# Kernel optimization log

Measured on AMD Instinct MI355X. Metric: run time of the kernel, lower is better.

Reference implementation:

```python
import jax, jax.numpy as jnp
import numpy as np

B, C, H, W = 8, 64, 128, 128
E, HEADS, HID = 3, 16, 16  # num experts, attention heads, routing hidden dim


def setup_inputs() -> dict:
    key = jax.random.key(0)
    ks = jax.random.split(key, 8)
    s = 0.05
    return {
        "x": jax.random.normal(ks[0], (B, C, H, W), jnp.float32),
        "hidden": jax.random.normal(ks[1], (B, HID, 1, 1), jnp.float32),
        # per-expert params, stacked along leading expert dim
        "qkv_w": jax.random.normal(ks[2], (E, 3 * C, C), jnp.float32) * s,   # 1x1 conv, no bias
        "dw_w": jax.random.normal(ks[3], (E, C, 1, 3, 3), jnp.float32) * s,  # depthwise 3x3
        "proj_w": jax.random.normal(ks[4], (E, C, C), jnp.float32) * s,      # 1x1 conv, no bias
        "temp": jnp.ones((E, HEADS, 1, 1), jnp.float32),                     # temperature
        # routing module params
        "r1_w": jax.random.normal(ks[5], (HID, C + HID), jnp.float32) * s,
        "r1_b": jnp.zeros((HID,), jnp.float32),
        "r3_w": jax.random.normal(ks[6], (E, HID), jnp.float32) * s,
        "r3_b": jnp.zeros((E,), jnp.float32),
    }


def _l2norm(t):
    # torch F.normalize: x / max(||x||, eps)
    n = jnp.sqrt(jnp.sum(t * t, axis=-1, keepdims=True))
    return t / jnp.maximum(n, 1e-12)


def _expert(x, qkv_w, dw_w, proj_w, temp):
    b, c, h, w = x.shape
    d = c // HEADS
    qkv = jnp.einsum('bchw,oc->bohw', x, qkv_w)  # [b,3c,h,w]
    q, k, v = jnp.split(qkv, 3, axis=1)
    rs = lambda t: t.reshape(b, HEADS, d, h * w)  # b head c (hw)
    q, k, v = _l2norm(rs(q)), _l2norm(rs(k)), rs(v)
    attn = jnp.einsum('bhcn,bhdn->bhcd', q, k) * temp  # tiny [b,head,d,d]
    attn = jax.nn.softmax(attn, axis=-1)
    out = jnp.einsum('bhcd,bhdn->bhcn', attn, v).reshape(b, c, h, w)
    out = jax.lax.conv_general_dilated(
        out, dw_w, window_strides=(1, 1), padding='SAME',
        feature_group_count=c, dimension_numbers=('NCHW', 'OIHW', 'NCHW'))
    return jnp.einsum('bchw,oc->bohw', out, proj_w)


def reference(x, hidden, qkv_w, dw_w, proj_w, temp, r1_w, r1_b, r3_w, r3_b):
    # routing
    x_global = jnp.mean(x, axis=(2, 3), keepdims=True)          # [b,c,1,1]
    cat = jnp.concatenate([x_global, hidden], axis=1)            # [b,c+16,1,1]
    h1 = jnp.einsum('bchw,oc->bohw', cat, r1_w) + r1_b[None, :, None, None]
    hidden_new = jax.nn.gelu(h1, approximate=False)              # [b,16,1,1]
    logit = jax.nn.relu(jnp.einsum('bchw,oc->bohw', hidden_new, r3_w)
                        + r3_b[None, :, None, None])             # [b,E,1,1]
    # dense expert evaluation
    outs = jnp.stack([_expert(x, qkv_w[i], dw_w[i], proj_w[i], temp[i])
                      for i in range(E)], axis=1)                # [b,E,c,h,w]
    logit5 = logit[..., None]                                    # [b,E,1,1,1]
    out = jnp.sum(outs * logit5, axis=1)                         # [b,c,h,w]
    return out, hidden_new, logit5
```

## Files before the change

kernel.cpp:

```cpp
#include <hip/hip_runtime.h>
#include <math.h>


#define OFF_XG    0
#define OFF_COV   512
#define OFF_LOGIT 33280
#define OFF_MV    33312
#define OFF_H_BYTES  526464
#define OFF_XT_BYTES 1116288

#define OUT_HID   8388608
#define OUT_LOGIT 8388736

#define XP 4224
#define HP 584

typedef __attribute__((ext_vector_type(8))) short bf16x8;
typedef __attribute__((ext_vector_type(4))) float f32x4;

__device__ inline unsigned short f2bf(float f) {
    union { float f; unsigned int u; } v; v.f = f;
    return (unsigned short)((v.u + 0x7FFFu + ((v.u >> 16) & 1u)) >> 16);
}
__device__ inline float bf2f(unsigned short h) {
    union { unsigned int u; float f; } v; v.u = ((unsigned int)h) << 16;
    return v.f;
}

__global__ __launch_bounds__(256) void cov_kernel(const float* __restrict__ x,
                                                  float* __restrict__ ws) {
    __shared__ unsigned short xl[64 * 520];
    const int t = threadIdx.x;
    const int w = t >> 6, l = t & 63;
    const int b = blockIdx.x >> 5;
    const int chunk = blockIdx.x & 31;
    const float* xb = x + ((size_t)b << 20) + (chunk << 9);

    for (int i = 0; i < 32; ++i) {
        const int idx = i * 256 + t;
        const int c = idx >> 7, u = idx & 127;
        const float4 v = *(const float4*)(xb + ((size_t)c << 14) + (u << 2));
        unsigned long long pk = (unsigned long long)f2bf(v.x)
                              | ((unsigned long long)f2bf(v.y) << 16)
                              | ((unsigned long long)f2bf(v.z) << 32)
                              | ((unsigned long long)f2bf(v.w) << 48);
        *(unsigned long long*)&xl[c * 520 + (u << 2)] = pk;
    }
    __syncthreads();

    {
        const int c = t & 63, q = t >> 6;
        float s = 0.f;
        for (int u = 0; u < 16; ++u) {
            const unsigned short* p = &xl[c * 520 + q * 128 + u * 8];
            #pragma unroll
            for (int j = 0; j < 8; ++j) s += bf2f(p[j]);
        }
        atomicAdd(ws + OFF_XG + b * 64 + c, s);
    }

    f32x4 acc[10];
    const f32x4 fz = {0.f, 0.f, 0.f, 0.f};
    #pragma unroll
    for (int q = 0; q < 10; ++q) acc[q] = fz;

    const int lane_a = (l & 15) * 520 + (l >> 4) * 8;
    #pragma unroll
    for (int ks = 0; ks < 4; ++ks) {
        const int p0 = w * 128 + ks * 32;
        bf16x8 fr[4];
        #pragma unroll
        for (int mi = 0; mi < 4; ++mi)
            fr[mi] = *(const bf16x8*)&xl[mi * 16 * 520 + p0 + lane_a];
        int q = 0;
        #pragma unroll
        for (int mi = 0; mi < 4; ++mi)
            #pragma unroll
            for (int ni = mi; ni < 4; ++ni) {
                acc[q] = __builtin_amdgcn_mfma_f32_16x16x32_bf16(fr[mi], fr[ni], acc[q], 0, 0, 0);
                ++q;
            }
    }

    {
        unsigned short* xtw = (unsigned short*)((char*)ws + OFF_XT_BYTES)
                            + ((size_t)b << 20) + ((size_t)(chunk << 9) << 6);
        for (int p = t; p < 512; p += 256) {
            #pragma unroll
            for (int i = 0; i < 8; ++i) {
                bf16x8 v;
                #pragma unroll
                for (int k = 0; k < 8; ++k) v[k] = (short)xl[(i * 8 + k) * 520 + p];
                *(bf16x8*)&xtw[((size_t)p << 6) + (i << 3)] = v;
            }
        }
    }
    __syncthreads();

    float* red = (float*)xl;
    #pragma unroll
    for (int q = 0; q < 10; ++q)
        #pragma unroll
        for (int j = 0; j < 4; ++j)
            red[w * 2560 + q * 256 + ((l >> 4) * 4 + j) * 16 + (l & 15)] = acc[q][j];
    __syncthreads();

    const int MI[10] = {0,0,0,0,1,1,1,2,2,3};
    const int NI[10] = {0,1,2,3,1,2,3,2,3,3};
    #pragma unroll
    for (int k = 0; k < 10; ++k) {
        const int i = k * 256 + t;
        const float s = red[i] + red[2560 + i] + red[5120 + i] + red[7680 + i];
        const int r = MI[k] * 16 + (t >> 4), c = NI[k] * 16 + (t & 15);
        atomicAdd(ws + OFF_COV + b * 4096 + r * 64 + c, s);
    }
}

__global__ __launch_bounds__(128) void route_kernel(const float* __restrict__ hidden,
        const float* __restrict__ r1w, const float* __restrict__ r1b,
        const float* __restrict__ r3w, const float* __restrict__ r3b,
        float* __restrict__ ws, float* __restrict__ out) {
    __shared__ float hn[128];
    const int t = threadIdx.x;
    {
        const int b = t >> 4, j = t & 15;
        const float* xg = ws + OFF_XG + b * 64;
        float s = r1b[j];
        for (int c = 0; c < 64; ++c) s += r1w[j*80 + c] * (xg[c] * (1.0f/16384.0f));
        for (int k = 0; k < 16; ++k) s += r1w[j*80 + 64 + k] * hidden[b*16 + k];
        float g = 0.5f * s * (1.0f + erff(s * 0.70710678118654752440f));
        hn[t] = g;
        out[OUT_HID + t] = g;
    }
    __syncthreads();
    if (t < 24) {
        const int b = t / 3, e = t - b * 3;
        float s = r3b[e];
        for (int j = 0; j < 16; ++j) s += r3w[e*16 + j] * hn[b*16 + j];
        s = fmaxf(s, 0.0f);
        ws[OFF_LOGIT + t] = s;
        out[OUT_LOGIT + t] = s;
    }
}

__global__ __launch_bounds__(256) void attn_kernel(const float* __restrict__ qkv_w,
        const float* __restrict__ temp, float* __restrict__ ws) {
    __shared__ float Wl[192 * 65];
    __shared__ float Cv[64 * 65];
    __shared__ float TQ[64 * 65];
    __shared__ float TK[64 * 65];
    __shared__ float qkb[256];
    __shared__ float qqb[64];
    __shared__ float kkb[64];
    __shared__ float atl[256];
    const int t = threadIdx.x;
    const int e = blockIdx.x >> 3, b = blockIdx.x & 7;
    const float lg = ws[OFF_LOGIT + b * 3 + e];
    if (!(lg > 0.0f)) return;

    for (int idx = t; idx < 12288; idx += 256)
        Wl[(idx >> 6) * 65 + (idx & 63)] = qkv_w[e * 12288 + idx];
    for (int idx = t; idx < 4096; idx += 256) {
        const int r = idx >> 6, c = idx & 63;
        const int rr = r < c ? r : c, cc = r < c ? c : r;
        Cv[r * 65 + c] = ws[OFF_COV + b * 4096 + rr * 64 + cc];
    }
    __syncthreads();

    {
        const int r = t >> 2, cq = (t & 3) << 4;
        float aq[16], ak[16];
        #pragma unroll
        for (int i = 0; i < 16; ++i) { aq[i] = 0.f; ak[i] = 0.f; }
        for (int c1 = 0; c1 < 64; ++c1) {
            float wq = Wl[r * 65 + c1];
            float wk = Wl[(64 + r) * 65 + c1];
            #pragma unroll
            for (int i = 0; i < 16; ++i) {
                float cv = Cv[c1 * 65 + cq + i];
                aq[i] += wq * cv; ak[i] += wk * cv;
            }
        }
        #pragma unroll
        for (int i = 0; i < 16; ++i) { TQ[r*65 + cq + i] = aq[i]; TK[r*65 + cq + i] = ak[i]; }
    }
    __syncthreads();

    for (int idx = t; idx < 384; idx += 256) {
        const int h = idx / 24, u = idx - h * 24;
        float s = 0.f;
        if (u < 16) {
            const int i = u >> 2, j = u & 3;
            const float* tq = &TQ[(4*h + i) * 65];
            const float* wk = &Wl[(64 + 4*h + j) * 65];
            for (int c = 0; c < 64; ++c) s += tq[c] * wk[c];
            qkb[h * 16 + u] = s;
        } else if (u < 20) {
            const int i = u - 16;
            const float* tq = &TQ[(4*h + i) * 65];
            const float* wq = &Wl[(4*h + i) * 65];
            for (int c = 0; c < 64; ++c) s += tq[c] * wq[c];
            qqb[h * 4 + i] = s;
        } else {
            const int j = u - 20;
            const float* tk = &TK[(4*h + j) * 65];
            const float* wk = &Wl[(64 + 4*h + j) * 65];
            for (int c = 0; c < 64; ++c) s += tk[c] * wk[c];
            kkb[h * 4 + j] = s;
        }
    }
    __syncthreads();

    if (t < 64) {
        const int h = t >> 2, i = t & 3;
        const float tp = temp[e * 16 + h];
        const float rq = 1.0f / fmaxf(sqrtf(qqb[h*4 + i]), 1e-12f);
        float lq[4];
        #pragma unroll
        for (int j = 0; j < 4; ++j) {
            float rk = 1.0f / fmaxf(sqrtf(kkb[h*4 + j]), 1e-12f);
            lq[j] = qkb[h*16 + i*4 + j] * rq * rk * tp;
        }
        float m = fmaxf(fmaxf(lq[0], lq[1]), fmaxf(lq[2], lq[3]));
        float ex[4]; float s = 0.f;
        #pragma unroll
        for (int j = 0; j < 4; ++j) { ex[j] = expf(lq[j] - m); s += ex[j]; }
        float inv = 1.0f / s;
        #pragma unroll
        for (int j = 0; j < 4; ++j) atl[h*16 + i*4 + j] = ex[j] * inv;
    }
    __syncthreads();

    float* mv = ws + OFF_MV + (size_t)blockIdx.x * 4096;
    for (int idx = t; idx < 4096; idx += 256) {
        const int o = idx >> 6, c = idx & 63;
        const int h = o >> 2, ii = o & 3;
        float s = 0.f;
        #pragma unroll
        for (int j = 0; j < 4; ++j)
            s += atl[h*16 + ii*4 + j] * Wl[(128 + 4*h + j) * 65 + c];
        mv[idx] = s;
    }
}

__global__ __launch_bounds__(256) void hbuild_kernel(const float* __restrict__ dw_w,
        const float* __restrict__ proj_w, float* __restrict__ ws) {
    __shared__ float Pl[64 * 65];
    __shared__ float Ml[64 * 65];
    const int t = threadIdx.x;
    const int b = blockIdx.x / 9, tap = blockIdx.x - b * 9;
    const int o = t >> 2, c4 = (t & 3) << 4;
    float s[16];
    #pragma unroll
    for (int i = 0; i < 16; ++i) s[i] = 0.f;
    for (int e = 0; e < 3; ++e) {
        const float lg = ws[OFF_LOGIT + b * 3 + e];
        __syncthreads();
        if (lg > 0.f) {
            for (int idx = t; idx < 4096; idx += 256) {
                const int oo = idx >> 6, mm = idx & 63;
                Pl[oo * 65 + mm] = proj_w[e * 4096 + idx] * dw_w[e * 576 + mm * 9 + tap] * lg;
                Ml[oo * 65 + mm] = ws[OFF_MV + (size_t)(e * 8 + b) * 4096 + idx];
            }
            __syncthreads();
            for (int m = 0; m < 64; ++m) {
                const float wv = Pl[o * 65 + m];
                const float* mr = &Ml[m * 65 + c4];
                #pragma unroll
                for (int i = 0; i < 16; ++i) s[i] += wv * mr[i];
            }
        }
    }
    unsigned short* Hg = (unsigned short*)((char*)ws + OFF_H_BYTES);
    unsigned short* hrow = Hg + (size_t)(b * 64 + o) * 576 + tap * 64 + c4;
    #pragma unroll
    for (int i = 0; i < 16; ++i) hrow[i] = f2bf(s[i]);
}

__global__ __launch_bounds__(512, 2) void conv_kernel(const float* __restrict__ ws_ro,
        float* __restrict__ out) {
    __shared__ unsigned short xl[10 * XP];
    __shared__ unsigned short hl[64 * HP];
    const int t = threadIdx.x;
    const int w = t >> 6, l = t & 63;
    const int bx = blockIdx.x;
    const int b = bx >> 5;
    const int tile = bx & 31;
    const int ty = tile >> 1, tx = tile & 1;
    const int y0 = ty << 3, x0 = tx << 6;
    const unsigned short* xt = (const unsigned short*)((const char*)ws_ro + OFF_XT_BYTES)
                             + ((size_t)b << 20);

    for (int rr = w; rr < 10; rr += 8) {
        const int gy = y0 - 1 + rr;
        const bool yok = ((unsigned)gy < 128u);
        for (int u = l; u < 528; u += 64) {
            const int col = u >> 3, j = u & 7;
            const int gx = x0 - 1 + col;
            bf16x8 v = {0, 0, 0, 0, 0, 0, 0, 0};
            if (yok && ((unsigned)gx < 128u))
                v = *(const bf16x8*)&xt[((size_t)((gy << 7) + gx) << 6) + (j << 3)];
            *(bf16x8*)&xl[rr * XP + (col << 6) + ((j ^ (col & 7)) << 3)] = v;
        }
    }
    {
        const unsigned short* hg = (const unsigned short*)((const char*)ws_ro + OFF_H_BYTES)
                                 + (size_t)b * 36864;
        #pragma unroll
        for (int r = 0; r < 8; ++r) {
            const int row = (w << 3) + r;
            for (int u = l; u < 72; u += 64)
                *(bf16x8*)&hl[row * HP + (u << 3)] = *(const bf16x8*)&hg[row * 576 + (u << 3)];
        }
    }
    __syncthreads();

    f32x4 acc[4][4];
    const f32x4 fz = {0.f, 0.f, 0.f, 0.f};
    #pragma unroll
    for (int mi = 0; mi < 4; ++mi)
        #pragma unroll
        for (int f = 0; f < 4; ++f) acc[mi][f] = fz;

    const int aoff = (l & 15) * HP + (l >> 4) * 8;
    const int bcol = (l & 15) * 64;
    int su8[3][2];
    #pragma unroll
    for (int dxi = 0; dxi < 3; ++dxi)
        #pragma unroll
        for (int s = 0; s < 2; ++s)
            su8[dxi][s] = ((s * 4 + (l >> 4)) ^ (((l & 15) + dxi) & 7)) << 3;

    #pragma unroll
    for (int tap = 0; tap < 9; ++tap) {
        const int dy = tap / 3 - 1;
        const int dxi = tap % 3;
        const int hr = w + 1 + dy;
        #pragma unroll
        for (int s = 0; s < 2; ++s) {
            const int k0 = tap * 64 + s * 32;
            bf16x8 af[4], bfr[4];
            #pragma unroll
            for (int mi = 0; mi < 4; ++mi)
                af[mi] = *(const bf16x8*)&hl[mi * 16 * HP + k0 + aoff];
            #pragma unroll
            for (int f = 0; f < 4; ++f)
                bfr[f] = *(const bf16x8*)&xl[hr * XP + (f * 16 + dxi) * 64 + bcol + su8[dxi][s]];
            #pragma unroll
            for (int mi = 0; mi < 4; ++mi)
                #pragma unroll
                for (int f = 0; f < 4; ++f)
                    acc[mi][f] = __builtin_amdgcn_mfma_f32_16x16x32_bf16(af[mi], bfr[f], acc[mi][f], 0, 0, 0);
        }
    }

    const int gy = y0 + w;
    float* ob = out + ((size_t)b << 20) + (gy << 7) + x0;
    const int orow = (l >> 4) << 2;
    const int ocol = l & 15;
    #pragma unroll
    for (int mi = 0; mi < 4; ++mi)
        #pragma unroll
        for (int f = 0; f < 4; ++f)
            #pragma unroll
            for (int j = 0; j < 4; ++j)
                ob[((size_t)(mi * 16 + orow + j) << 14) + f * 16 + ocol] = acc[mi][f][j];
}

extern "C" void kernel_launch(void* const* d_in, const int* in_sizes, int n_in,
                              void* d_out, int out_size, void* d_ws, size_t ws_size,
                              hipStream_t stream) {
    const float* x      = (const float*)d_in[0];
    const float* hidden = (const float*)d_in[1];
    const float* qkv_w  = (const float*)d_in[2];
    const float* dw_w   = (const float*)d_in[3];
    const float* proj_w = (const float*)d_in[4];
    const float* temp   = (const float*)d_in[5];
    const float* r1w    = (const float*)d_in[6];
    const float* r1b    = (const float*)d_in[7];
    const float* r3w    = (const float*)d_in[8];
    const float* r3b    = (const float*)d_in[9];
    float* out = (float*)d_out;
    float* ws  = (float*)d_ws;

    hipMemsetAsync(ws, 0, (size_t)(512 + 32768) * sizeof(float), stream);

    cov_kernel   <<<dim3(256), dim3(256), 0, stream>>>(x, ws);
    route_kernel <<<dim3(1),   dim3(128), 0, stream>>>(hidden, r1w, r1b, r3w, r3b, ws, out);
    attn_kernel  <<<dim3(24),  dim3(256), 0, stream>>>(qkv_w, temp, ws);
    hbuild_kernel<<<dim3(72),  dim3(256), 0, stream>>>(dw_w, proj_w, ws);
    conv_kernel  <<<dim3(256), dim3(512), 0, stream>>>(ws, out);
}
```

Baseline: 177.2 us.

## Replace atomic covariance reduction with per-block partials and fuse routing into attention

The covariance and channel-mean accumulation now write per-block partial sums to workspace instead of issuing global atomics, which removes the memset and atomic contention. The attention kernel reduces the 32 partials per batch itself and recomputes the routing MLP per block, so the separate route kernel launch goes away. In exchange, each attention block reads 32x2560 partial floats, and the routing math is done redundantly across experts. Workspace offsets are enlarged to hold the partials.

Result: no change. 176.8 us (-0.2%).

```diff
diff --git a/kernel.cpp b/kernel.cpp
--- a/kernel.cpp
+++ b/kernel.cpp
@@ -2,12 +2,12 @@
 #include <math.h>
 
 
-#define OFF_XG    0
-#define OFF_COV   512
-#define OFF_LOGIT 33280
-#define OFF_MV    33312
-#define OFF_H_BYTES  526464
-#define OFF_XT_BYTES 1116288
+#define OFF_PART  0
+#define OFF_XGP   655360
+#define OFF_LOGIT 671744
+#define OFF_MV    671776
+#define OFF_H_BYTES  3080320
+#define OFF_XT_BYTES 3670144
 
 #define OUT_HID   8388608
 #define OUT_LOGIT 8388736
@@ -30,6 +30,7 @@
 __global__ __launch_bounds__(256) void cov_kernel(const float* __restrict__ x,
                                                   float* __restrict__ ws) {
     __shared__ unsigned short xl[64 * 520];
+    __shared__ float xgq[256];
     const int t = threadIdx.x;
     const int w = t >> 6, l = t & 63;
     const int b = blockIdx.x >> 5;
@@ -56,7 +57,7 @@
             #pragma unroll
             for (int j = 0; j < 8; ++j) s += bf2f(p[j]);
         }
-        atomicAdd(ws + OFF_XG + b * 64 + c, s);
+        xgq[q * 64 + c] = s;
     }
 
     f32x4 acc[10];
@@ -105,46 +106,19 @@
             red[w * 2560 + q * 256 + ((l >> 4) * 4 + j) * 16 + (l & 15)] = acc[q][j];
     __syncthreads();
 
-    const int MI[10] = {0,0,0,0,1,1,1,2,2,3};
-    const int NI[10] = {0,1,2,3,1,2,3,2,3,3};
-    #pragma unroll
-    for (int k = 0; k < 10; ++k) {
-        const int i = k * 256 + t;
-        const float s = red[i] + red[2560 + i] + red[5120 + i] + red[7680 + i];
-        const int r = MI[k] * 16 + (t >> 4), c = NI[k] * 16 + (t & 15);
-        atomicAdd(ws + OFF_COV + b * 4096 + r * 64 + c, s);
-    }
-}
-
-__global__ __launch_bounds__(128) void route_kernel(const float* __restrict__ hidden,
+    float* part = ws + OFF_PART + (size_t)blockIdx.x * 2560;
+    for (int i = t; i < 2560; i += 256)
+        part[i] = (red[i] + red[2560 + i]) + (red[5120 + i] + red[7680 + i]);
+    if (t < 64)
+        ws[OFF_XGP + blockIdx.x * 64 + t] =
+            (xgq[t] + xgq[64 + t]) + (xgq[128 + t] + xgq[192 + t]);
+}
+
+__global__ __launch_bounds__(256) void attn_kernel(const float* __restrict__ qkv_w,
+        const float* __restrict__ temp, const float* __restrict__ hidden,
         const float* __restrict__ r1w, const float* __restrict__ r1b,
         const float* __restrict__ r3w, const float* __restrict__ r3b,
         float* __restrict__ ws, float* __restrict__ out) {
-    __shared__ float hn[128];
-    const int t = threadIdx.x;
-    {
-        const int b = t >> 4, j = t & 15;
-        const float* xg = ws + OFF_XG + b * 64;
-        float s = r1b[j];
-        for (int c = 0; c < 64; ++c) s += r1w[j*80 + c] * (xg[c] * (1.0f/16384.0f));
-        for (int k = 0; k < 16; ++k) s += r1w[j*80 + 64 + k] * hidden[b*16 + k];
-        float g = 0.5f * s * (1.0f + erff(s * 0.70710678118654752440f));
-        hn[t] = g;
-        out[OUT_HID + t] = g;
-    }
-    __syncthreads();
-    if (t < 24) {
-        const int b = t / 3, e = t - b * 3;
-        float s = r3b[e];
-        for (int j = 0; j < 16; ++j) s += r3w[e*16 + j] * hn[b*16 + j];
-        s = fmaxf(s, 0.0f);
-        ws[OFF_LOGIT + t] = s;
-        out[OUT_LOGIT + t] = s;
-    }
-}
-
-__global__ __launch_bounds__(256) void attn_kernel(const float* __restrict__ qkv_w,
-        const float* __restrict__ temp, float* __restrict__ ws) {
     __shared__ float Wl[192 * 65];
     __shared__ float Cv[64 * 65];
     __shared__ float TQ[64 * 65];
@@ -153,17 +127,53 @@
     __shared__ float qqb[64];
     __shared__ float kkb[64];
     __shared__ float atl[256];
+    __shared__ float xg[64];
+    __shared__ float hn[16];
+    __shared__ float lgl[3];
     const int t = threadIdx.x;
     const int e = blockIdx.x >> 3, b = blockIdx.x & 7;
-    const float lg = ws[OFF_LOGIT + b * 3 + e];
+
+    if (t < 64) {
+        const float* xgp = ws + OFF_XGP + (b * 32) * 64;
+        float s = 0.f;
+        for (int k = 0; k < 32; ++k) s += xgp[k * 64 + t];
+        xg[t] = s;
+    }
+    __syncthreads();
+    if (t < 16) {
+        float s = r1b[t];
+        for (int c = 0; c < 64; ++c) s += r1w[t*80 + c] * (xg[c] * (1.0f/16384.0f));
+        for (int k = 0; k < 16; ++k) s += r1w[t*80 + 64 + k] * hidden[b*16 + k];
+        float g = 0.5f * s * (1.0f + erff(s * 0.70710678118654752440f));
+        hn[t] = g;
+        if (e == 0) out[OUT_HID + b * 16 + t] = g;
+    }
+    __syncthreads();
+    if (t < 3) {
+        float s = r3b[t];
+        for (int j = 0; j < 16; ++j) s += r3w[t*16 + j] * hn[j];
+        s = fmaxf(s, 0.0f);
+        lgl[t] = s;
+        if (e == 0) { ws[OFF_LOGIT + b * 3 + t] = s; out[OUT_LOGIT + b * 3 + t] = s; }
+    }
+    __syncthreads();
+    const float lg = lgl[e];
     if (!(lg > 0.0f)) return;
 
     for (int idx = t; idx < 12288; idx += 256)
         Wl[(idx >> 6) * 65 + (idx & 63)] = qkv_w[e * 12288 + idx];
-    for (int idx = t; idx < 4096; idx += 256) {
-        const int r = idx >> 6, c = idx & 63;
-        const int rr = r < c ? r : c, cc = r < c ? c : r;
-        Cv[r * 65 + c] = ws[OFF_COV + b * 4096 + rr * 64 + cc];
+    {
+        const int MI[10] = {0,0,0,0,1,1,1,2,2,3};
+        const int NI[10] = {0,1,2,3,1,2,3,2,3,3};
+        const float* part = ws + OFF_PART + (size_t)(b * 32) * 2560;
+        for (int idx = t; idx < 2560; idx += 256) {
+            float s = 0.f;
+            for (int k = 0; k < 32; ++k) s += part[(size_t)k * 2560 + idx];
+            const int q = idx >> 8, i = idx & 255;
+            const int r = MI[q] * 16 + (i >> 4), c = NI[q] * 16 + (i & 15);
+            Cv[r * 65 + c] = s;
+            Cv[c * 65 + r] = s;
+        }
     }
     __syncthreads();
 
@@ -383,11 +393,9 @@
     float* out = (float*)d_out;
     float* ws  = (float*)d_ws;
 
-    hipMemsetAsync(ws, 0, (size_t)(512 + 32768) * sizeof(float), stream);
-
     cov_kernel   <<<dim3(256), dim3(256), 0, stream>>>(x, ws);
-    route_kernel <<<dim3(1),   dim3(128), 0, stream>>>(hidden, r1w, r1b, r3w, r3b, ws, out);
-    attn_kernel  <<<dim3(24),  dim3(256), 0, stream>>>(qkv_w, temp, ws);
+    attn_kernel  <<<dim3(24),  dim3(256), 0, stream>>>(qkv_w, temp, hidden,
+                                                       r1w, r1b, r3w, r3b, ws, out);
     hbuild_kernel<<<dim3(72),  dim3(256), 0, stream>>>(dw_w, proj_w, ws);
     conv_kernel  <<<dim3(256), dim3(512), 0, stream>>>(ws, out);
 }
```
